# Optimization experiments

Measured on AMD Instinct MI355X. Metric: run time of the kernel, lower is better.

Reference implementation:

```python
import jax, jax.numpy as jnp
import numpy as np

NEG_SLOPE = 0.01  # F.leaky_relu default
EPS = 1e-12       # F.normalize default eps


def neigh_agg(x, edges, num_node, W, b):
    # x: [N, D]; edges: [2, E] (src, tgt); returns [num_node, D]
    src, tgt = edges[0], edges[1]
    h = jax.nn.relu(x @ W + b)                 # [N, D]
    msgs = h[tgt]                              # [E, D] gather
    aggr = jax.ops.segment_sum(msgs, src, num_segments=num_node)  # scatter-add
    deg = jax.ops.segment_sum(jnp.ones(src.shape, h.dtype), src, num_segments=num_node)
    deg = jnp.clip(deg, 1.0)                   # clamp(min=1)
    return aggr / deg[:, None]                 # dropout omitted (eval mode)


def setup_inputs() -> dict:
    key = jax.random.key(0)
    ks = jax.random.split(key, 20)
    N, D, E = 50000, 128, 1600000
    inp = {}
    for i, r in enumerate("gdcs"):
        inp[f"x_{r}"] = jax.random.normal(ks[i], (N, D), jnp.float32)
        inp[f"edges_{r}"] = jax.random.randint(ks[4 + i], (2, E), 0, N, jnp.int32)
    inp["x_node"] = jax.random.normal(ks[8], (N, D), jnp.float32)
    inp["num_node"] = N
    s = 1.0 / np.sqrt(D)
    for i, r in enumerate("gdcs"):
        inp[f"W_{r}"] = jax.random.uniform(ks[9 + 2 * i], (D, D), jnp.float32, -s, s)
        inp[f"b_{r}"] = jax.random.uniform(ks[10 + 2 * i], (D,), jnp.float32, -s, s)
    inp["u"] = jax.random.normal(ks[17], (2 * D, 1), jnp.float32)
    s2 = 1.0 / np.sqrt(2 * D)
    inp["W_lin"] = jax.random.uniform(ks[18], (2 * D, D), jnp.float32, -s2, s2)
    inp["b_lin"] = jax.random.uniform(ks[19], (D,), jnp.float32, -s2, s2)
    return inp


def reference(x_g, x_d, x_c, x_s, edges_g, edges_d, edges_c, edges_s, x_node,
              num_node, W_g, b_g, W_d, b_d, W_c, b_c, W_s, b_s, u, W_lin, b_lin):
    aggrs = [
        neigh_agg(x_g, edges_g, num_node, W_g, b_g),
        neigh_agg(x_d, edges_d, num_node, W_d, b_d),
        neigh_agg(x_c, edges_c, num_node, W_c, b_c),
        neigh_agg(x_s, edges_s, num_node, W_s, b_s),
    ]
    # attention scores per relation: exp(leaky_relu([aggr, x_node] @ u))
    scores = [jnp.exp(jax.nn.leaky_relu(jnp.concatenate([a, x_node], axis=-1) @ u,
                                        NEG_SLOPE)) for a in aggrs]  # each [N,1]
    denom = scores[0] + scores[1] + scores[2] + scores[3]
    combined = sum((s / denom) * a for s, a in zip(scores, aggrs))   # [N, D]
    y = jax.nn.relu(jnp.concatenate([x_node, combined], axis=-1) @ W_lin + b_lin)
    norm = jnp.maximum(jnp.linalg.norm(y, axis=-1, keepdims=True), EPS)
    return y / norm
```

## Files before the change

kernel.cpp:

```cpp
#include <hip/hip_runtime.h>
#include <hip/hip_fp16.h>
#include <cstddef>


#define BN1       512
#define BN1_SHIFT 9
#define BCAP1     20480
#define NB1MAX    128
#define BLK_E     16384

struct IP4 { const int* p[4]; };
struct FP4 { const float* p[4]; };

typedef _Float16 half8 __attribute__((ext_vector_type(8)));
typedef float f32x4 __attribute__((ext_vector_type(4)));
typedef float f32x2 __attribute__((ext_vector_type(2)));

__global__ __launch_bounds__(256) void prep0_k(FP4 Wm, const float* __restrict__ Wl,
                                               __half* __restrict__ Wt,
                                               __half* __restrict__ Wlt,
                                               int* __restrict__ bcur, int nzero) {
    const int b = blockIdx.x, t = threadIdx.x;
    if (b < 256) {
        int r = b >> 6;
        int i = (b & 63) * 256 + t;
        int k = i & 127, c = i >> 7;
        Wt[(size_t)r * 16384 + c * 128 + k] = __float2half(Wm.p[r][(size_t)k * 128 + c]);
    } else if (b < 384) {
        int i = (b - 256) * 256 + t;
        int k = i & 255, c = i >> 8;
        Wlt[(size_t)c * 256 + k] = __float2half(Wl[(size_t)k * 128 + c]);
    } else {
        for (int i = (b - 384) * 256 + t; i < nzero; i += 64 * 256) bcur[i] = 0;
    }
}

__global__ __launch_bounds__(256) void binGemm_k(IP4 ed, int4 Ev, int* __restrict__ bcur,
                                                 int* __restrict__ staging, int nb1, int binb,
                                                 FP4 X, const __half* __restrict__ Wt,
                                                 FP4 Bv, unsigned char* __restrict__ H8,
                                                 int M, int gb) {
    __shared__ int ldsu[4096];
    const int t = threadIdx.x;
    const int x = blockIdx.x;

    if (x < 4 * binb) {
        const int r = x / binb;
        const int bx = x - r * binb;
        const int E = (r == 0) ? Ev.x : (r == 1) ? Ev.y : (r == 2) ? Ev.z : Ev.w;
        const int e0 = bx * BLK_E;
        if (e0 >= E) return;
        const int e1 = min(e0 + BLK_E, E);
        const int* es = ed.p[r];
        const int* et = es + E;
        int* bc = bcur + (size_t)r * nb1 * 16;
        int* stg = staging + (size_t)r * nb1 * BCAP1;
        int* hist = ldsu;
        int* curs = ldsu + NB1MAX;

        for (int b = t; b < nb1; b += 256) hist[b] = 0;
        __syncthreads();
        {
            const int n = e1 - e0;
            const int n4 = n >> 2;
            const int4* s4 = reinterpret_cast<const int4*>(es + e0);
            for (int i = t; i < n4; i += 256) {
                int4 s = s4[i];
                atomicAdd(&hist[s.x >> BN1_SHIFT], 1);
                atomicAdd(&hist[s.y >> BN1_SHIFT], 1);
                atomicAdd(&hist[s.z >> BN1_SHIFT], 1);
                atomicAdd(&hist[s.w >> BN1_SHIFT], 1);
            }
            for (int i = e0 + n4 * 4 + t; i < e1; i += 256)
                atomicAdd(&hist[es[i] >> BN1_SHIFT], 1);
        }
        __syncthreads();
        for (int b = t; b < nb1; b += 256) {
            int c = hist[b];
            curs[b] = c ? atomicAdd(&bc[b * 16], c) : 0;
        }
        __syncthreads();
        {
            const int n = e1 - e0;
            const int n4 = n >> 2;
            const int4* s4 = reinterpret_cast<const int4*>(es + e0);
            const int4* t4 = reinterpret_cast<const int4*>(et + e0);
            for (int i = t; i < n4; i += 256) {
                int4 s = s4[i];
                int4 tg = t4[i];
                int b, p;
                b = s.x >> BN1_SHIFT; p = atomicAdd(&curs[b], 1);
                if (p < BCAP1) stg[(size_t)b * BCAP1 + p] = ((s.x & 511) << 16) | tg.x;
                b = s.y >> BN1_SHIFT; p = atomicAdd(&curs[b], 1);
                if (p < BCAP1) stg[(size_t)b * BCAP1 + p] = ((s.y & 511) << 16) | tg.y;
                b = s.z >> BN1_SHIFT; p = atomicAdd(&curs[b], 1);
                if (p < BCAP1) stg[(size_t)b * BCAP1 + p] = ((s.z & 511) << 16) | tg.z;
                b = s.w >> BN1_SHIFT; p = atomicAdd(&curs[b], 1);
                if (p < BCAP1) stg[(size_t)b * BCAP1 + p] = ((s.w & 511) << 16) | tg.w;
            }
            for (int i = e0 + n4 * 4 + t; i < e1; i += 256) {
                int s = es[i];
                int b = s >> BN1_SHIFT;
                int p = atomicAdd(&curs[b], 1);
                if (p < BCAP1) stg[(size_t)b * BCAP1 + p] = ((s & 511) << 16) | et[i];
            }
        }
    } else {
        const int g = x - 4 * binb;
        const int r = g / gb;
        const int bx = g - r * gb;
        const float* A = X.p[r];
        const __half* Wr = Wt + (size_t)r * 16384;
        const float* bias = Bv.p[r];
        unsigned char* Hr = H8 + (size_t)r * M * 128;
        const int n0 = bx * 64;
        char* AsB = reinterpret_cast<char*>(ldsu);

        for (int s = t; s < 1024; s += 256) {
            int row = s >> 4, c8 = (s & 15) << 3;
            int grow = n0 + row;
            float4 v0 = make_float4(0.f, 0.f, 0.f, 0.f), v1 = v0;
            if (grow < M) {
                v0 = *reinterpret_cast<const float4*>(&A[(size_t)grow * 128 + c8]);
                v1 = *reinterpret_cast<const float4*>(&A[(size_t)grow * 128 + c8 + 4]);
            }
            half8 hv;
            hv[0] = (_Float16)v0.x; hv[1] = (_Float16)v0.y;
            hv[2] = (_Float16)v0.z; hv[3] = (_Float16)v0.w;
            hv[4] = (_Float16)v1.x; hv[5] = (_Float16)v1.y;
            hv[6] = (_Float16)v1.z; hv[7] = (_Float16)v1.w;
            int byte = (row * 256 + c8 * 2) ^ ((row & 7) << 4);
            *reinterpret_cast<half8*>(AsB + byte) = hv;
        }
        __syncthreads();

        const int w = t >> 6, lane = t & 63;
        const int r0 = (w & 1) * 32, c0 = (w >> 1) * 64;
        const int lr = lane & 15;
        const int lk = (lane >> 4) * 8;

        f32x4 acc[2][4] = {};
        #pragma unroll
        for (int k0 = 0; k0 < 128; k0 += 32) {
            half8 af[2], bf[4];
            #pragma unroll
            for (int mi = 0; mi < 2; ++mi) {
                int row = r0 + mi * 16 + lr;
                int byte = (row * 256 + (k0 + lk) * 2) ^ ((row & 7) << 4);
                af[mi] = *reinterpret_cast<const half8*>(AsB + byte);
            }
            #pragma unroll
            for (int ni = 0; ni < 4; ++ni) {
                int col = c0 + ni * 16 + lr;
                bf[ni] = *reinterpret_cast<const half8*>(&Wr[(size_t)col * 128 + k0 + lk]);
            }
            #pragma unroll
            for (int mi = 0; mi < 2; ++mi)
                #pragma unroll
                for (int ni = 0; ni < 4; ++ni)
                    acc[mi][ni] = __builtin_amdgcn_mfma_f32_16x16x32_f16(af[mi], bf[ni],
                                                                         acc[mi][ni], 0, 0, 0);
        }
        __syncthreads();
        unsigned char* ht = reinterpret_cast<unsigned char*>(AsB);
        #pragma unroll
        for (int ni = 0; ni < 4; ++ni) {
            int col = c0 + ni * 16 + lr;
            float bb = bias[col];
            #pragma unroll
            for (int mi = 0; mi < 2; ++mi) {
                #pragma unroll
                for (int j = 0; j < 4; ++j) {
                    int row = r0 + mi * 16 + (lane >> 4) * 4 + j;
                    float y = fmaxf(acc[mi][ni][j] + bb, 0.f);
                    int e = __builtin_amdgcn_cvt_pk_fp8_f32(y, 0.f, 0, false);
                    ht[row * 128 + col] = (unsigned char)e;
                }
            }
        }
        __syncthreads();
        {
            int row = t >> 2, cb = (t & 3) * 32;
            int grow = n0 + row;
            if (grow < M) {
                const int4* p = reinterpret_cast<const int4*>(ht + row * 128 + cb);
                int4 a = p[0], b = p[1];
                int4* q = reinterpret_cast<int4*>(Hr + (size_t)grow * 128 + cb);
                q[0] = a; q[1] = b;
            }
        }
    }
}

__global__ __launch_bounds__(256) void csr2_k(const int* __restrict__ staging,
                                              const int* __restrict__ bcur,
                                              int* __restrict__ gcur,
                                              int2* __restrict__ offc,
                                              unsigned short* __restrict__ sorted,
                                              int nb1, int N) {
    const int r = blockIdx.y;
    const int b = blockIdx.x;
    const int gi = r * nb1 + b;
    const int sz = min(bcur[(size_t)gi * 16], BCAP1);
    const int* stg = staging + (size_t)gi * BCAP1;
    const int nbase = b * BN1;
    const int t = threadIdx.x;
    const int lane = t & 63, wid = t >> 6;

    __shared__ int hist[BN1];
    __shared__ int cur[BN1];
    __shared__ int wsum[4];
    __shared__ int base_s;

    if (t == 0) base_s = atomicAdd(gcur, sz);
    hist[t] = 0;
    hist[t + 256] = 0;
    __syncthreads();
    {
        const int sz4 = sz >> 2;
        const int4* s4 = reinterpret_cast<const int4*>(stg);
        for (int i = t; i < sz4; i += 256) {
            int4 v = s4[i];
            atomicAdd(&hist[((unsigned)v.x) >> 16], 1);
            atomicAdd(&hist[((unsigned)v.y) >> 16], 1);
            atomicAdd(&hist[((unsigned)v.z) >> 16], 1);
            atomicAdd(&hist[((unsigned)v.w) >> 16], 1);
        }
        for (int i = sz4 * 4 + t; i < sz; i += 256)
            atomicAdd(&hist[((unsigned)stg[i]) >> 16], 1);
    }
    __syncthreads();
    const int base = base_s;
    int v0 = hist[2 * t], v1 = hist[2 * t + 1];
    int ps = v0 + v1;
    int incl = ps;
    #pragma unroll
    for (int d = 1; d < 64; d <<= 1) {
        int x = __shfl_up(incl, d);
        if (lane >= d) incl += x;
    }
    if (lane == 63) wsum[wid] = incl;
    __syncthreads();
    if (t == 0) {
        int a = 0;
        #pragma unroll
        for (int i = 0; i < 4; ++i) { int x = wsum[i]; wsum[i] = a; a += x; }
    }
    __syncthreads();
    int e0 = wsum[wid] + incl - ps;
    cur[2 * t] = e0;
    cur[2 * t + 1] = e0 + v0;
    {
        int n0 = nbase + 2 * t;
        if (n0 < N) offc[(size_t)r * N + n0] = make_int2(base + e0, v0);
        if (n0 + 1 < N) offc[(size_t)r * N + n0 + 1] = make_int2(base + e0 + v0, v1);
    }
    __syncthreads();
    {
        const int sz4 = sz >> 2;
        const int4* s4 = reinterpret_cast<const int4*>(stg);
        for (int i = t; i < sz4; i += 256) {
            int4 v = s4[i];
            int p;
            p = atomicAdd(&cur[((unsigned)v.x) >> 16], 1);
            sorted[base + p] = (unsigned short)(v.x & 0xFFFF);
            p = atomicAdd(&cur[((unsigned)v.y) >> 16], 1);
            sorted[base + p] = (unsigned short)(v.y & 0xFFFF);
            p = atomicAdd(&cur[((unsigned)v.z) >> 16], 1);
            sorted[base + p] = (unsigned short)(v.z & 0xFFFF);
            p = atomicAdd(&cur[((unsigned)v.w) >> 16], 1);
            sorted[base + p] = (unsigned short)(v.w & 0xFFFF);
        }
        for (int i = sz4 * 4 + t; i < sz; i += 256) {
            int rec = stg[i];
            int p = atomicAdd(&cur[((unsigned)rec) >> 16], 1);
            sorted[base + p] = (unsigned short)(rec & 0xFFFF);
        }
    }
}

__global__ __launch_bounds__(256) void gather_attn_k(const unsigned char* __restrict__ H8,
                                                     const float* __restrict__ xn,
                                                     const float* __restrict__ u,
                                                     const int2* __restrict__ offc,
                                                     const unsigned short* __restrict__ sorted,
                                                     __half* __restrict__ comb, int N) {
    const int node = blockIdx.x * 4 + (threadIdx.x >> 6);
    if (node >= N) return;
    const int lane = threadIdx.x & 63;
    const int q = lane >> 4;
    const int c = lane & 15;

    float2 x2 = *reinterpret_cast<const float2*>(&xn[(size_t)node * 128 + lane * 2]);
    float2 ux = *reinterpret_cast<const float2*>(&u[128 + lane * 2]);
    float px = x2.x * ux.x + x2.y * ux.y;
    #pragma unroll
    for (int m = 1; m < 64; m <<= 1) px += __shfl_xor(px, m);

    float4 ua0 = reinterpret_cast<const float4*>(u)[c * 2];
    float4 ua1 = reinterpret_cast<const float4*>(u)[c * 2 + 1];

    float a[4][8];
    float invd[4], pr[4];
    #pragma unroll
    for (int r = 0; r < 4; ++r) {
        const int2 oc = offc[(size_t)r * N + node];
        const int beg = oc.x, cnt = oc.y;
        const unsigned char* hr = H8 + (size_t)r * N * 128;
        const unsigned short* sl = sorted + beg;
        f32x2 s01 = {0.f, 0.f}, s23 = {0.f, 0.f}, s45 = {0.f, 0.f}, s67 = {0.f, 0.f};
        int my = (lane < cnt) ? (int)sl[lane] : 0;
        for (int j0 = 0; j0 < cnt; j0 += 64) {
            const int m = min(64, cnt - j0);
            int my_next = (j0 + 64 + lane < cnt) ? (int)sl[j0 + 64 + lane] : 0;
            int j = 0;
            for (; j + 8 <= m; j += 8) {
                int tg0 = __shfl(my, j + q);
                int tg1 = __shfl(my, j + q + 4);
                uint2 raw0 = reinterpret_cast<const uint2*>(hr + (size_t)tg0 * 128)[c];
                uint2 raw1 = reinterpret_cast<const uint2*>(hr + (size_t)tg1 * 128)[c];
                s01 += __builtin_amdgcn_cvt_pk_f32_fp8((int)raw0.x, false);
                s23 += __builtin_amdgcn_cvt_pk_f32_fp8((int)raw0.x, true);
                s45 += __builtin_amdgcn_cvt_pk_f32_fp8((int)raw0.y, false);
                s67 += __builtin_amdgcn_cvt_pk_f32_fp8((int)raw0.y, true);
                s01 += __builtin_amdgcn_cvt_pk_f32_fp8((int)raw1.x, false);
                s23 += __builtin_amdgcn_cvt_pk_f32_fp8((int)raw1.x, true);
                s45 += __builtin_amdgcn_cvt_pk_f32_fp8((int)raw1.y, false);
                s67 += __builtin_amdgcn_cvt_pk_f32_fp8((int)raw1.y, true);
            }
            for (; j < m; j += 4) {
                int jj = j + q;
                int tg = __shfl(my, min(jj, m - 1));
                if (jj < m) {
                    uint2 raw = reinterpret_cast<const uint2*>(hr + (size_t)tg * 128)[c];
                    s01 += __builtin_amdgcn_cvt_pk_f32_fp8((int)raw.x, false);
                    s23 += __builtin_amdgcn_cvt_pk_f32_fp8((int)raw.x, true);
                    s45 += __builtin_amdgcn_cvt_pk_f32_fp8((int)raw.y, false);
                    s67 += __builtin_amdgcn_cvt_pk_f32_fp8((int)raw.y, true);
                }
            }
            my = my_next;
        }
        float s[8] = {s01[0], s01[1], s23[0], s23[1], s45[0], s45[1], s67[0], s67[1]};
        #pragma unroll
        for (int k = 0; k < 8; ++k) {
            s[k] += __shfl_xor(s[k], 16);
            s[k] += __shfl_xor(s[k], 32);
        }
        float dp = s[0] * ua0.x + s[1] * ua0.y + s[2] * ua0.z + s[3] * ua0.w
                 + s[4] * ua1.x + s[5] * ua1.y + s[6] * ua1.z + s[7] * ua1.w;
        #pragma unroll
        for (int m = 1; m < 16; m <<= 1) dp += __shfl_xor(dp, m);
        pr[r] = dp;
        invd[r] = 1.0f / fmaxf((float)cnt, 1.0f);
        #pragma unroll
        for (int k = 0; k < 8; ++k) a[r][k] = s[k];
    }
    float wgt[4], denom = 0.f;
    #pragma unroll
    for (int r = 0; r < 4; ++r) {
        float sc = pr[r] * invd[r] + px;
        float z = (sc > 0.f) ? sc : 0.01f * sc;
        wgt[r] = expf(z);
        denom += wgt[r];
    }
    float cf[4];
    #pragma unroll
    for (int r = 0; r < 4; ++r) cf[r] = (wgt[r] / denom) * invd[r];
    if (q == 0) {
        half8 o;
        #pragma unroll
        for (int k = 0; k < 8; ++k)
            o[k] = (_Float16)(cf[0] * a[0][k] + cf[1] * a[1][k] +
                              cf[2] * a[2][k] + cf[3] * a[3][k]);
        *reinterpret_cast<half8*>(&comb[(size_t)node * 128 + c * 8]) = o;
    }
}

__global__ __launch_bounds__(256) void gemm_out_k(const float* __restrict__ Xn,
                                                  const __half* __restrict__ Cb,
                                                  const __half* __restrict__ Wlt,
                                                  const float* __restrict__ bias,
                                                  float* __restrict__ out, int M) {
    __shared__ __half As[64 * 128];
    __shared__ float rowss[64];
    const int t = threadIdx.x;
    const int n0 = blockIdx.x * 64;
    char* AsB = reinterpret_cast<char*>(As);
    if (t < 64) rowss[t] = 0.f;

    const int w = t >> 6, lane = t & 63;
    const int r0 = (w & 1) * 32, c0 = (w >> 1) * 64;
    const int lr = lane & 15;
    const int lk = (lane >> 4) * 8;

    f32x4 acc[2][4] = {};
    #pragma unroll
    for (int p = 0; p < 2; ++p) {
        if (p == 0) {
            for (int s = t; s < 1024; s += 256) {
                int row = s >> 4, c8 = (s & 15) << 3;
                int grow = n0 + row;
                float4 v0 = make_float4(0.f, 0.f, 0.f, 0.f), v1 = v0;
                if (grow < M) {
                    v0 = *reinterpret_cast<const float4*>(&Xn[(size_t)grow * 128 + c8]);
                    v1 = *reinterpret_cast<const float4*>(&Xn[(size_t)grow * 128 + c8 + 4]);
                }
                half8 hv;
                hv[0] = (_Float16)v0.x; hv[1] = (_Float16)v0.y;
                hv[2] = (_Float16)v0.z; hv[3] = (_Float16)v0.w;
                hv[4] = (_Float16)v1.x; hv[5] = (_Float16)v1.y;
                hv[6] = (_Float16)v1.z; hv[7] = (_Float16)v1.w;
                int byte = (row * 256 + c8 * 2) ^ ((row & 7) << 4);
                *reinterpret_cast<half8*>(AsB + byte) = hv;
            }
        } else {
            for (int s = t; s < 1024; s += 256) {
                int row = s >> 4, c8 = (s & 15) << 3;
                int grow = n0 + row;
                half8 hv = {};
                if (grow < M) hv = *reinterpret_cast<const half8*>(&Cb[(size_t)grow * 128 + c8]);
                int byte = (row * 256 + c8 * 2) ^ ((row & 7) << 4);
                *reinterpret_cast<half8*>(AsB + byte) = hv;
            }
        }
        __syncthreads();
        #pragma unroll
        for (int k0 = 0; k0 < 128; k0 += 32) {
            half8 af[2], bf[4];
            #pragma unroll
            for (int mi = 0; mi < 2; ++mi) {
                int row = r0 + mi * 16 + lr;
                int byte = (row * 256 + (k0 + lk) * 2) ^ ((row & 7) << 4);
                af[mi] = *reinterpret_cast<const half8*>(AsB + byte);
            }
            #pragma unroll
            for (int ni = 0; ni < 4; ++ni) {
                int col = c0 + ni * 16 + lr;
                bf[ni] = *reinterpret_cast<const half8*>(&Wlt[(size_t)col * 256 + p * 128 + k0 + lk]);
            }
            #pragma unroll
            for (int mi = 0; mi < 2; ++mi)
                #pragma unroll
                for (int ni = 0; ni < 4; ++ni)
                    acc[mi][ni] = __builtin_amdgcn_mfma_f32_16x16x32_f16(af[mi], bf[ni],
                                                                         acc[mi][ni], 0, 0, 0);
        }
        __syncthreads();
    }
    float bbv[4];
    #pragma unroll
    for (int ni = 0; ni < 4; ++ni) bbv[ni] = bias[c0 + ni * 16 + lr];
    #pragma unroll
    for (int mi = 0; mi < 2; ++mi) {
        #pragma unroll
        for (int j = 0; j < 4; ++j) {
            int row_l = r0 + mi * 16 + (lane >> 4) * 4 + j;
            float ss = 0.f;
            #pragma unroll
            for (int ni = 0; ni < 4; ++ni) {
                float y = fmaxf(acc[mi][ni][j] + bbv[ni], 0.f);
                ss += y * y;
            }
            ss += __shfl_xor(ss, 1); ss += __shfl_xor(ss, 2);
            ss += __shfl_xor(ss, 4); ss += __shfl_xor(ss, 8);
            if (lr == 0) atomicAdd(&rowss[row_l], ss);
        }
    }
    __syncthreads();
    #pragma unroll
    for (int mi = 0; mi < 2; ++mi) {
        #pragma unroll
        for (int j = 0; j < 4; ++j) {
            int row_l = r0 + mi * 16 + (lane >> 4) * 4 + j;
            int grow = n0 + row_l;
            if (grow < M) {
                float inv = 1.0f / fmaxf(sqrtf(rowss[row_l]), 1e-12f);
                #pragma unroll
                for (int ni = 0; ni < 4; ++ni) {
                    float y = fmaxf(acc[mi][ni][j] + bbv[ni], 0.f);
                    out[(size_t)grow * 128 + c0 + ni * 16 + lr] = y * inv;
                }
            }
        }
    }
}

extern "C" void kernel_launch(void* const* d_in, const int* in_sizes, int n_in,
                              void* d_out, int out_size, void* d_ws, size_t ws_size,
                              hipStream_t stream) {
    FP4 X  = {{(const float*)d_in[0], (const float*)d_in[2],
               (const float*)d_in[4], (const float*)d_in[6]}};
    IP4 ED = {{(const int*)d_in[1], (const int*)d_in[3],
               (const int*)d_in[5], (const int*)d_in[7]}};
    const float* xn = (const float*)d_in[8];
    FP4 Wm = {{(const float*)d_in[10], (const float*)d_in[12],
               (const float*)d_in[14], (const float*)d_in[16]}};
    FP4 Bv = {{(const float*)d_in[11], (const float*)d_in[13],
               (const float*)d_in[15], (const float*)d_in[17]}};
    const float* u  = (const float*)d_in[18];
    const float* Wl = (const float*)d_in[19];
    const float* bl = (const float*)d_in[20];
    float* out = (float*)d_out;

    const int N = in_sizes[8] / 128;
    int E[4];
    for (int r = 0; r < 4; ++r) E[r] = in_sizes[1 + 2 * r] / 2;
    const int4 Ev = make_int4(E[0], E[1], E[2], E[3]);
    const int nb1 = (N + BN1 - 1) / BN1;
    int maxE = 0;
    for (int r = 0; r < 4; ++r) maxE = (E[r] > maxE) ? E[r] : maxE;

    unsigned char* h8 = (unsigned char*)d_ws;
    char*  ubase   = (char*)(h8 + (size_t)4 * N * 128);
    int*   staging = (int*)ubase;
    __half* comb   = (__half*)ubase;
    size_t usz = (size_t)4 * nb1 * BCAP1 * sizeof(int);
    size_t csz = (size_t)N * 128 * sizeof(__half);
    char*  after   = ubase + (usz > csz ? usz : csz);
    __half* Wt     = (__half*)after;
    __half* Wlt    = Wt + (size_t)4 * 16384;
    int2* offc   = (int2*)(Wlt + (size_t)128 * 256);
    int* bcur    = (int*)(offc + (size_t)4 * N);
    int* gcur    = bcur + (size_t)4 * nb1 * 16;
    unsigned short* sorted = (unsigned short*)(gcur + 16);

    const int gb = (N + 63) / 64;
    const int binb = (maxE + BLK_E - 1) / BLK_E;

    prep0_k<<<448, 256, 0, stream>>>(Wm, Wl, Wt, Wlt, bcur, 4 * nb1 * 16 + 16);
    binGemm_k<<<4 * binb + 4 * gb, 256, 0, stream>>>(ED, Ev, bcur, staging, nb1, binb,
                                                     X, Wt, Bv, h8, N, gb);
    csr2_k<<<dim3(nb1, 4), 256, 0, stream>>>(staging, bcur, gcur, offc, sorted, nb1, N);
    gather_attn_k<<<(N + 3) / 4, 256, 0, stream>>>(h8, xn, u, offc, sorted, comb, N);
    gemm_out_k<<<gb, 256, 0, stream>>>(xn, comb, Wlt, bl, out, N);
}
```

Baseline: 303.5 us.

## Fuse neighbor gather/attention with output GEMM via shared-memory combined tile

Merges the gather+attention kernel and the output linear kernel into one. Each block of 4 waves processes 64 nodes, 16 per wave, and writes the fp16 combined features straight into a swizzled shared-memory tile, which then feeds the MFMA GEMM directly. This removes the global round trip of the combined buffer and one kernel launch. In exchange the grid shrinks from N/4 blocks to N/64, with each wave looping serially over 16 nodes, which may reduce the parallelism available to hide the latency of the irregular gathers.

```diff
diff --git a/kernel.cpp b/kernel.cpp
--- a/kernel.cpp
+++ b/kernel.cpp
@@ -279,174 +279,184 @@
     }
 }
 
-__global__ __launch_bounds__(256) void gather_attn_k(const unsigned char* __restrict__ H8,
-                                                     const float* __restrict__ xn,
-                                                     const float* __restrict__ u,
-                                                     const int2* __restrict__ offc,
-                                                     const unsigned short* __restrict__ sorted,
-                                                     __half* __restrict__ comb, int N) {
-    const int node = blockIdx.x * 4 + (threadIdx.x >> 6);
-    if (node >= N) return;
-    const int lane = threadIdx.x & 63;
-    const int q = lane >> 4;
-    const int c = lane & 15;
-
-    float2 x2 = *reinterpret_cast<const float2*>(&xn[(size_t)node * 128 + lane * 2]);
-    float2 ux = *reinterpret_cast<const float2*>(&u[128 + lane * 2]);
-    float px = x2.x * ux.x + x2.y * ux.y;
-    #pragma unroll
-    for (int m = 1; m < 64; m <<= 1) px += __shfl_xor(px, m);
-
-    float4 ua0 = reinterpret_cast<const float4*>(u)[c * 2];
-    float4 ua1 = reinterpret_cast<const float4*>(u)[c * 2 + 1];
-
-    float a[4][8];
-    float invd[4], pr[4];
-    #pragma unroll
-    for (int r = 0; r < 4; ++r) {
-        const int2 oc = offc[(size_t)r * N + node];
-        const int beg = oc.x, cnt = oc.y;
-        const unsigned char* hr = H8 + (size_t)r * N * 128;
-        const unsigned short* sl = sorted + beg;
-        f32x2 s01 = {0.f, 0.f}, s23 = {0.f, 0.f}, s45 = {0.f, 0.f}, s67 = {0.f, 0.f};
-        int my = (lane < cnt) ? (int)sl[lane] : 0;
-        for (int j0 = 0; j0 < cnt; j0 += 64) {
-            const int m = min(64, cnt - j0);
-            int my_next = (j0 + 64 + lane < cnt) ? (int)sl[j0 + 64 + lane] : 0;
-            int j = 0;
-            for (; j + 8 <= m; j += 8) {
-                int tg0 = __shfl(my, j + q);
-                int tg1 = __shfl(my, j + q + 4);
-                uint2 raw0 = reinterpret_cast<const uint2*>(hr + (size_t)tg0 * 128)[c];
-                uint2 raw1 = reinterpret_cast<const uint2*>(hr + (size_t)tg1 * 128)[c];
-                s01 += __builtin_amdgcn_cvt_pk_f32_fp8((int)raw0.x, false);
-                s23 += __builtin_amdgcn_cvt_pk_f32_fp8((int)raw0.x, true);
-                s45 += __builtin_amdgcn_cvt_pk_f32_fp8((int)raw0.y, false);
-                s67 += __builtin_amdgcn_cvt_pk_f32_fp8((int)raw0.y, true);
-                s01 += __builtin_amdgcn_cvt_pk_f32_fp8((int)raw1.x, false);
-                s23 += __builtin_amdgcn_cvt_pk_f32_fp8((int)raw1.x, true);
-                s45 += __builtin_amdgcn_cvt_pk_f32_fp8((int)raw1.y, false);
-                s67 += __builtin_amdgcn_cvt_pk_f32_fp8((int)raw1.y, true);
-            }
-            for (; j < m; j += 4) {
-                int jj = j + q;
-                int tg = __shfl(my, min(jj, m - 1));
-                if (jj < m) {
-                    uint2 raw = reinterpret_cast<const uint2*>(hr + (size_t)tg * 128)[c];
-                    s01 += __builtin_amdgcn_cvt_pk_f32_fp8((int)raw.x, false);
-                    s23 += __builtin_amdgcn_cvt_pk_f32_fp8((int)raw.x, true);
-                    s45 += __builtin_amdgcn_cvt_pk_f32_fp8((int)raw.y, false);
-                    s67 += __builtin_amdgcn_cvt_pk_f32_fp8((int)raw.y, true);
-                }
-            }
-            my = my_next;
-        }
-        float s[8] = {s01[0], s01[1], s23[0], s23[1], s45[0], s45[1], s67[0], s67[1]};
-        #pragma unroll
-        for (int k = 0; k < 8; ++k) {
-            s[k] += __shfl_xor(s[k], 16);
-            s[k] += __shfl_xor(s[k], 32);
-        }
-        float dp = s[0] * ua0.x + s[1] * ua0.y + s[2] * ua0.z + s[3] * ua0.w
-                 + s[4] * ua1.x + s[5] * ua1.y + s[6] * ua1.z + s[7] * ua1.w;
-        #pragma unroll
-        for (int m = 1; m < 16; m <<= 1) dp += __shfl_xor(dp, m);
-        pr[r] = dp;
-        invd[r] = 1.0f / fmaxf((float)cnt, 1.0f);
-        #pragma unroll
-        for (int k = 0; k < 8; ++k) a[r][k] = s[k];
-    }
-    float wgt[4], denom = 0.f;
-    #pragma unroll
-    for (int r = 0; r < 4; ++r) {
-        float sc = pr[r] * invd[r] + px;
-        float z = (sc > 0.f) ? sc : 0.01f * sc;
-        wgt[r] = expf(z);
-        denom += wgt[r];
-    }
-    float cf[4];
-    #pragma unroll
-    for (int r = 0; r < 4; ++r) cf[r] = (wgt[r] / denom) * invd[r];
-    if (q == 0) {
-        half8 o;
-        #pragma unroll
-        for (int k = 0; k < 8; ++k)
-            o[k] = (_Float16)(cf[0] * a[0][k] + cf[1] * a[1][k] +
-                              cf[2] * a[2][k] + cf[3] * a[3][k]);
-        *reinterpret_cast<half8*>(&comb[(size_t)node * 128 + c * 8]) = o;
-    }
-}
-
-__global__ __launch_bounds__(256) void gemm_out_k(const float* __restrict__ Xn,
-                                                  const __half* __restrict__ Cb,
-                                                  const __half* __restrict__ Wlt,
-                                                  const float* __restrict__ bias,
-                                                  float* __restrict__ out, int M) {
-    __shared__ __half As[64 * 128];
+__global__ __launch_bounds__(256) void gatherGemm_k(const unsigned char* __restrict__ H8,
+                                                    const float* __restrict__ xn,
+                                                    const float* __restrict__ u,
+                                                    const int2* __restrict__ offc,
+                                                    const unsigned short* __restrict__ sorted,
+                                                    const __half* __restrict__ Wlt,
+                                                    const float* __restrict__ bias,
+                                                    float* __restrict__ out, int N) {
+    __shared__ __half Cs[64 * 128];
     __shared__ float rowss[64];
     const int t = threadIdx.x;
     const int n0 = blockIdx.x * 64;
-    char* AsB = reinterpret_cast<char*>(As);
+    char* CsB = reinterpret_cast<char*>(Cs);
+    const int w = t >> 6, lane = t & 63;
+    const int q = lane >> 4;
+    const int c = lane & 15;
     if (t < 64) rowss[t] = 0.f;
 
-    const int w = t >> 6, lane = t & 63;
+    float4 ua0 = reinterpret_cast<const float4*>(u)[c * 2];
+    float4 ua1 = reinterpret_cast<const float4*>(u)[c * 2 + 1];
+    float2 ux = *reinterpret_cast<const float2*>(&u[128 + lane * 2]);
+
+    #pragma unroll 1
+    for (int ln = w * 16; ln < w * 16 + 16; ++ln) {
+        const int node = n0 + ln;
+        const int byteo = (ln * 256 + c * 16) ^ ((ln & 7) << 4);
+        if (node < N) {
+            float2 x2 = *reinterpret_cast<const float2*>(&xn[(size_t)node * 128 + lane * 2]);
+            float px = x2.x * ux.x + x2.y * ux.y;
+            #pragma unroll
+            for (int m = 1; m < 64; m <<= 1) px += __shfl_xor(px, m);
+
+            float a[4][8];
+            float invd[4], pr[4];
+            #pragma unroll
+            for (int r = 0; r < 4; ++r) {
+                const int2 oc = offc[(size_t)r * N + node];
+                const int beg = oc.x, cnt = oc.y;
+                const unsigned char* hr = H8 + (size_t)r * N * 128;
+                const unsigned short* sl = sorted + beg;
+                f32x2 s01 = {0.f, 0.f}, s23 = {0.f, 0.f}, s45 = {0.f, 0.f}, s67 = {0.f, 0.f};
+                int my = (lane < cnt) ? (int)sl[lane] : 0;
+                for (int j0 = 0; j0 < cnt; j0 += 64) {
+                    const int m = min(64, cnt - j0);
+                    int my_next = (j0 + 64 + lane < cnt) ? (int)sl[j0 + 64 + lane] : 0;
+                    int j = 0;
+                    for (; j + 8 <= m; j += 8) {
+                        int tg0 = __shfl(my, j + q);
+                        int tg1 = __shfl(my, j + q + 4);
+                        uint2 raw0 = reinterpret_cast<const uint2*>(hr + (size_t)tg0 * 128)[c];
+                        uint2 raw1 = reinterpret_cast<const uint2*>(hr + (size_t)tg1 * 128)[c];
+                        s01 += __builtin_amdgcn_cvt_pk_f32_fp8((int)raw0.x, false);
+                        s23 += __builtin_amdgcn_cvt_pk_f32_fp8((int)raw0.x, true);
+                        s45 += __builtin_amdgcn_cvt_pk_f32_fp8((int)raw0.y, false);
+                        s67 += __builtin_amdgcn_cvt_pk_f32_fp8((int)raw0.y, true);
+                        s01 += __builtin_amdgcn_cvt_pk_f32_fp8((int)raw1.x, false);
+                        s23 += __builtin_amdgcn_cvt_pk_f32_fp8((int)raw1.x, true);
+                        s45 += __builtin_amdgcn_cvt_pk_f32_fp8((int)raw1.y, false);
+                        s67 += __builtin_amdgcn_cvt_pk_f32_fp8((int)raw1.y, true);
+                    }
+                    for (; j < m; j += 4) {
+                        int jj = j + q;
+                        int tg = __shfl(my, min(jj, m - 1));
+                        if (jj < m) {
+                            uint2 raw = reinterpret_cast<const uint2*>(hr + (size_t)tg * 128)[c];
+                            s01 += __builtin_amdgcn_cvt_pk_f32_fp8((int)raw.x, false);
+                            s23 += __builtin_amdgcn_cvt_pk_f32_fp8((int)raw.x, true);
+                            s45 += __builtin_amdgcn_cvt_pk_f32_fp8((int)raw.y, false);
+                            s67 += __builtin_amdgcn_cvt_pk_f32_fp8((int)raw.y, true);
+                        }
+                    }
+                    my = my_next;
+                }
+                float s[8] = {s01[0], s01[1], s23[0], s23[1], s45[0], s45[1], s67[0], s67[1]};
+                #pragma unroll
+                for (int k = 0; k < 8; ++k) {
+                    s[k] += __shfl_xor(s[k], 16);
+                    s[k] += __shfl_xor(s[k], 32);
+                }
+                float dp = s[0] * ua0.x + s[1] * ua0.y + s[2] * ua0.z + s[3] * ua0.w
+                         + s[4] * ua1.x + s[5] * ua1.y + s[6] * ua1.z + s[7] * ua1.w;
+                #pragma unroll
+                for (int m = 1; m < 16; m <<= 1) dp += __shfl_xor(dp, m);
+                pr[r] = dp;
+                invd[r] = 1.0f / fmaxf((float)cnt, 1.0f);
+                #pragma unroll
+                for (int k = 0; k < 8; ++k) a[r][k] = s[k];
+            }
+            float wgt[4], denom = 0.f;
+            #pragma unroll
+            for (int r = 0; r < 4; ++r) {
+                float sc = pr[r] * invd[r] + px;
+                float z = (sc > 0.f) ? sc : 0.01f * sc;
+                wgt[r] = expf(z);
+                denom += wgt[r];
+            }
+            float cf[4];
+            #pragma unroll
+            for (int r = 0; r < 4; ++r) cf[r] = (wgt[r] / denom) * invd[r];
+            if (q == 0) {
+                half8 o;
+                #pragma unroll
+                for (int k = 0; k < 8; ++k)
+                    o[k] = (_Float16)(cf[0] * a[0][k] + cf[1] * a[1][k] +
+                                      cf[2] * a[2][k] + cf[3] * a[3][k]);
+                *reinterpret_cast<half8*>(CsB + byteo) = o;
+            }
+        } else if (q == 0) {
+            half8 z = {};
+            *reinterpret_cast<half8*>(CsB + byteo) = z;
+        }
+    }
+    __syncthreads();
+
     const int r0 = (w & 1) * 32, c0 = (w >> 1) * 64;
     const int lr = lane & 15;
     const int lk = (lane >> 4) * 8;
 
     f32x4 acc[2][4] = {};
     #pragma unroll
-    for (int p = 0; p < 2; ++p) {
-        if (p == 0) {
-            for (int s = t; s < 1024; s += 256) {
-                int row = s >> 4, c8 = (s & 15) << 3;
-                int grow = n0 + row;
-                float4 v0 = make_float4(0.f, 0.f, 0.f, 0.f), v1 = v0;
-                if (grow < M) {
-                    v0 = *reinterpret_cast<const float4*>(&Xn[(size_t)grow * 128 + c8]);
-                    v1 = *reinterpret_cast<const float4*>(&Xn[(size_t)grow * 128 + c8 + 4]);
-                }
-                half8 hv;
-                hv[0] = (_Float16)v0.x; hv[1] = (_Float16)v0.y;
-                hv[2] = (_Float16)v0.z; hv[3] = (_Float16)v0.w;
-                hv[4] = (_Float16)v1.x; hv[5] = (_Float16)v1.y;
-                hv[6] = (_Float16)v1.z; hv[7] = (_Float16)v1.w;
-                int byte = (row * 256 + c8 * 2) ^ ((row & 7) << 4);
-                *reinterpret_cast<half8*>(AsB + byte) = hv;
-            }
-        } else {
-            for (int s = t; s < 1024; s += 256) {
-                int row = s >> 4, c8 = (s & 15) << 3;
-                int grow = n0 + row;
-                half8 hv = {};
-                if (grow < M) hv = *reinterpret_cast<const half8*>(&Cb[(size_t)grow * 128 + c8]);
-                int byte = (row * 256 + c8 * 2) ^ ((row & 7) << 4);
-                *reinterpret_cast<half8*>(AsB + byte) = hv;
-            }
-        }
-        __syncthreads();
-        #pragma unroll
-        for (int k0 = 0; k0 < 128; k0 += 32) {
-            half8 af[2], bf[4];
-            #pragma unroll
-            for (int mi = 0; mi < 2; ++mi) {
-                int row = r0 + mi * 16 + lr;
-                int byte = (row * 256 + (k0 + lk) * 2) ^ ((row & 7) << 4);
-                af[mi] = *reinterpret_cast<const half8*>(AsB + byte);
-            }
-            #pragma unroll
-            for (int ni = 0; ni < 4; ++ni) {
-                int col = c0 + ni * 16 + lr;
-                bf[ni] = *reinterpret_cast<const half8*>(&Wlt[(size_t)col * 256 + p * 128 + k0 + lk]);
-            }
-            #pragma unroll
-            for (int mi = 0; mi < 2; ++mi)
-                #pragma unroll
-                for (int ni = 0; ni < 4; ++ni)
-                    acc[mi][ni] = __builtin_amdgcn_mfma_f32_16x16x32_f16(af[mi], bf[ni],
-                                                                         acc[mi][ni], 0, 0, 0);
-        }
-        __syncthreads();
+    for (int k0 = 0; k0 < 128; k0 += 32) {
+        half8 af[2], bf[4];
+        #pragma unroll
+        for (int mi = 0; mi < 2; ++mi) {
+            int row = r0 + mi * 16 + lr;
+            int byte = (row * 256 + (k0 + lk) * 2) ^ ((row & 7) << 4);
+            af[mi] = *reinterpret_cast<const half8*>(CsB + byte);
+        }
+        #pragma unroll
+        for (int ni = 0; ni < 4; ++ni) {
+            int col = c0 + ni * 16 + lr;
+            bf[ni] = *reinterpret_cast<const half8*>(&Wlt[(size_t)col * 256 + 128 + k0 + lk]);
+        }
+        #pragma unroll
+        for (int mi = 0; mi < 2; ++mi)
+            #pragma unroll
+            for (int ni = 0; ni < 4; ++ni)
+                acc[mi][ni] = __builtin_amdgcn_mfma_f32_16x16x32_f16(af[mi], bf[ni],
+                                                                     acc[mi][ni], 0, 0, 0);
+    }
+    __syncthreads();
+    for (int s = t; s < 1024; s += 256) {
+        int row = s >> 4, c8 = (s & 15) << 3;
+        int grow = n0 + row;
+        float4 v0 = make_float4(0.f, 0.f, 0.f, 0.f), v1 = v0;
+        if (grow < N) {
+            v0 = *reinterpret_cast<const float4*>(&xn[(size_t)grow * 128 + c8]);
+            v1 = *reinterpret_cast<const float4*>(&xn[(size_t)grow * 128 + c8 + 4]);
+        }
+        half8 hv;
+        hv[0] = (_Float16)v0.x; hv[1] = (_Float16)v0.y;
+        hv[2] = (_Float16)v0.z; hv[3] = (_Float16)v0.w;
+        hv[4] = (_Float16)v1.x; hv[5] = (_Float16)v1.y;
+        hv[6] = (_Float16)v1.z; hv[7] = (_Float16)v1.w;
+        int byte = (row * 256 + c8 * 2) ^ ((row & 7) << 4);
+        *reinterpret_cast<half8*>(CsB + byte) = hv;
+    }
+    __syncthreads();
+    #pragma unroll
+    for (int k0 = 0; k0 < 128; k0 += 32) {
+        half8 af[2], bf[4];
+        #pragma unroll
+        for (int mi = 0; mi < 2; ++mi) {
+            int row = r0 + mi * 16 + lr;
+            int byte = (row * 256 + (k0 + lk) * 2) ^ ((row & 7) << 4);
+            af[mi] = *reinterpret_cast<const half8*>(CsB + byte);
+        }
+        #pragma unroll
+        for (int ni = 0; ni < 4; ++ni) {
+            int col = c0 + ni * 16 + lr;
+            bf[ni] = *reinterpret_cast<const half8*>(&Wlt[(size_t)col * 256 + k0 + lk]);
+        }
+        #pragma unroll
+        for (int mi = 0; mi < 2; ++mi)
+            #pragma unroll
+            for (int ni = 0; ni < 4; ++ni)
+                acc[mi][ni] = __builtin_amdgcn_mfma_f32_16x16x32_f16(af[mi], bf[ni],
+                                                                     acc[mi][ni], 0, 0, 0);
     }
     float bbv[4];
     #pragma unroll
@@ -474,7 +484,7 @@
         for (int j = 0; j < 4; ++j) {
             int row_l = r0 + mi * 16 + (lane >> 4) * 4 + j;
             int grow = n0 + row_l;
-            if (grow < M) {
+            if (grow < N) {
                 float inv = 1.0f / fmaxf(sqrtf(rowss[row_l]), 1e-12f);
                 #pragma unroll
                 for (int ni = 0; ni < 4; ++ni) {
@@ -512,13 +522,8 @@
     for (int r = 0; r < 4; ++r) maxE = (E[r] > maxE) ? E[r] : maxE;
 
     unsigned char* h8 = (unsigned char*)d_ws;
-    char*  ubase   = (char*)(h8 + (size_t)4 * N * 128);
-    int*   staging = (int*)ubase;
-    __half* comb   = (__half*)ubase;
-    size_t usz = (size_t)4 * nb1 * BCAP1 * sizeof(int);
-    size_t csz = (size_t)N * 128 * sizeof(__half);
-    char*  after   = ubase + (usz > csz ? usz : csz);
-    __half* Wt     = (__half*)after;
+    int*   staging = (int*)(h8 + (size_t)4 * N * 128);
+    __half* Wt     = (__half*)(staging + (size_t)4 * nb1 * BCAP1);
     __half* Wlt    = Wt + (size_t)4 * 16384;
     int2* offc   = (int2*)(Wlt + (size_t)128 * 256);
     int* bcur    = (int*)(offc + (size_t)4 * N);
@@ -532,6 +537,5 @@
     binGemm_k<<<4 * binb + 4 * gb, 256, 0, stream>>>(ED, Ev, bcur, staging, nb1, binb,
                                                      X, Wt, Bv, h8, N, gb);
     csr2_k<<<dim3(nb1, 4), 256, 0, stream>>>(staging, bcur, gcur, offc, sorted, nb1, N);
-    gather_attn_k<<<(N + 3) / 4, 256, 0, stream>>>(h8, xn, u, offc, sorted, comb, N);
-    gemm_out_k<<<gb, 256, 0, stream>>>(xn, comb, Wlt, bl, out, N);
+    gatherGemm_k<<<gb, 256, 0, stream>>>(h8, xn, u, offc, sorted, Wlt, bl, out, N);
 }
```

Result: slower. 516.0 us (+70.1%).
